# Performance work log

Hardware: AMD Instinct MI355X
Metric: run time of the kernel (lower is better)

The kernel has to match this reference:

```python
import jax, jax.numpy as jnp
import numpy as np

NEG_SLOPE = 0.2


def _gat(x, edge_index, W, a_src, a_dst, b):
    """PyG-style GATConv, heads=1, add_self_loops=True."""
    n = x.shape[0]
    x = x @ W  # [n, out]
    loops = jnp.arange(n, dtype=edge_index.dtype)
    src = jnp.concatenate([edge_index[0], loops])
    dst = jnp.concatenate([edge_index[1], loops])
    a_s = x @ a_src  # [n]
    a_d = x @ a_dst  # [n]
    e = jax.nn.leaky_relu(a_s[src] + a_d[dst], NEG_SLOPE)  # [E]
    m = jax.ops.segment_max(e, dst, num_segments=n)  # stable softmax per dst
    ex = jnp.exp(e - m[dst])
    denom = jax.ops.segment_sum(ex, dst, num_segments=n)
    alpha = ex / denom[dst]
    out = jax.ops.segment_sum(alpha[:, None] * x[src], dst, num_segments=n)
    return out + b


def _lin(key, fan_in, fan_out):
    k1, k2 = jax.random.split(key)
    s = 1.0 / np.sqrt(fan_in)
    W = jax.random.uniform(k1, (fan_in, fan_out), jnp.float32, -s, s)
    b = jax.random.uniform(k2, (fan_out,), jnp.float32, -s, s)
    return W, b


def setup_inputs() -> dict:
    key = jax.random.key(0)
    ks = jax.random.split(key, 24)
    ND, FD = 50000, 128   # drug nodes / feat dim
    NC, FC = 10000, 735   # cell nodes / feat dim
    ED, EC = 800000, 160000
    B = 16384
    inp = {}
    inp['drug_x'] = jax.random.normal(ks[0], (ND, FD), jnp.float32)
    inp['cell_x'] = jax.random.normal(ks[1], (NC, FC), jnp.float32)
    inp['drug_edge_index'] = jax.random.randint(ks[2], (2, ED), 0, ND, jnp.int64 if jax.config.jax_enable_x64 else jnp.int32)
    inp['cell_edge_index'] = jax.random.randint(ks[3], (2, EC), 0, NC, jnp.int32)
    inp['drug_indices'] = jax.random.randint(ks[4], (B,), 0, ND, jnp.int32)
    inp['cell_indices'] = jax.random.randint(ks[5], (B,), 0, NC, jnp.int32)
    # drug feature transform: Linear(128,256)
    inp['dW1'], inp['db1'] = _lin(ks[6], FD, 256)
    # cell feature transform: Linear(735,1024) -> Linear(1024,256)
    inp['cW1'], inp['cb1'] = _lin(ks[7], FC, 1024)
    inp['cW2'], inp['cb2'] = _lin(ks[8], 1024, 256)
    # drug GAT (256->256)
    inp['gdW'], _ = _lin(ks[9], 256, 256)
    inp['gdas'] = jax.random.normal(ks[10], (256,), jnp.float32) * 0.1
    inp['gdad'] = jax.random.normal(ks[11], (256,), jnp.float32) * 0.1
    inp['gdb'] = jnp.zeros((256,), jnp.float32)
    # cell GAT1 (256->1024)
    inp['g1W'], _ = _lin(ks[12], 256, 1024)
    inp['g1as'] = jax.random.normal(ks[13], (1024,), jnp.float32) * 0.1
    inp['g1ad'] = jax.random.normal(ks[14], (1024,), jnp.float32) * 0.1
    inp['g1b'] = jnp.zeros((1024,), jnp.float32)
    # cell GAT2 (1024->256)
    inp['g2W'], _ = _lin(ks[15], 1024, 256)
    inp['g2as'] = jax.random.normal(ks[16], (256,), jnp.float32) * 0.1
    inp['g2ad'] = jax.random.normal(ks[17], (256,), jnp.float32) * 0.1
    inp['g2b'] = jnp.zeros((256,), jnp.float32)
    inp['rW1'], inp['rb1'] = _lin(ks[18], 512, 512)
    inp['rW2'], inp['rb2'] = _lin(ks[19], 512, 512)
    inp['rW3'], inp['rb3'] = _lin(ks[20], 512, 1)
    return inp


def reference(drug_x, cell_x, drug_edge_index, cell_edge_index, drug_indices, cell_indices,
              dW1, db1, cW1, cb1, cW2, cb2,
              gdW, gdas, gdad, gdb,
              g1W, g1as, g1ad, g1b,
              g2W, g2as, g2ad, g2b,
              rW1, rb1, rW2, rb2, rW3, rb3):
    # feature transforms (dropout = identity in eval mode)
    d = jax.nn.relu(drug_x @ dW1 + db1)                 # [ND, 256]
    c = jax.nn.relu(cell_x @ cW1 + cb1)                 # [NC, 1024]
    c = jax.nn.relu(c @ cW2 + cb2)                      # [NC, 256]
    # GAT layers
    d = jax.nn.relu(_gat(d, drug_edge_index, gdW, gdas, gdad, gdb))   # [ND, 256]
    c = jax.nn.relu(_gat(c, cell_edge_index, g1W, g1as, g1ad, g1b))   # [NC, 1024]
    c = jax.nn.relu(_gat(c, cell_edge_index, g2W, g2as, g2ad, g2b))   # [NC, 256]
    comb = jnp.concatenate([d[drug_indices], c[cell_indices]], axis=-1)  # [B, 512]
    h = jax.nn.elu(comb @ rW1 + rb1)
    h = jax.nn.elu(h @ rW2 + rb2)
    return h @ rW3 + rb3                                 # [B, 1]
```

## Files before the change

kernel.cpp:

```cpp
#include <hip/hip_runtime.h>
#include <math.h>

#define NEG_SLOPE 0.2f

typedef __attribute__((ext_vector_type(8))) short short8;
typedef __attribute__((ext_vector_type(4))) float floatx4;

__device__ __forceinline__ unsigned short f2bf(float f) {
    unsigned u = __float_as_uint(f);
    u += 0x7fffu + ((u >> 16) & 1u);
    return (unsigned short)(u >> 16);
}
__device__ __forceinline__ float bf2f(unsigned short h) {
    return __uint_as_float((unsigned)h << 16);
}
__device__ __forceinline__ float lrelu(float v) {
    return v > 0.f ? v : NEG_SLOPE * v;
}

typedef __attribute__((address_space(3))) unsigned int lds_u32;
typedef const __attribute__((address_space(1))) unsigned int glb_u32c;
__device__ __forceinline__ void gll16(const unsigned short* g, unsigned short* l) {
    __builtin_amdgcn_global_load_lds((glb_u32c*)g, (lds_u32*)l, 16, 0, 0);
}

struct SJob { const float* W; unsigned short* Th; unsigned short* Tl; int K, N, Kp, base; };
struct SJobs { SJob j[8]; };

__global__ __launch_bounds__(256) void split_transpose_multi(SJobs js) {
    int t = blockIdx.x;
    int ji = 0;
#pragma unroll
    for (int q = 1; q < 8; ++q) if (t >= js.j[q].base) ji = q;
    const SJob jb = js.j[ji];
    int local = t - jb.base;
    int ntiles = jb.N / 32;
    int tn = local % ntiles, tk = local / ntiles;
    int k0 = tk * 32, n0 = tn * 32;
    __shared__ float tbuf[32][33];
    int c = threadIdx.x & 31, r = threadIdx.x >> 5;
    for (int rr = r; rr < 32; rr += 8) {
        int k = k0 + rr, n = n0 + c;
        tbuf[rr][c] = (k < jb.K && n < jb.N) ? jb.W[(long)k * jb.N + n] : 0.f;
    }
    __syncthreads();
    for (int rr = r; rr < 32; rr += 8) {
        int n = n0 + rr, k = k0 + c;
        if (n < jb.N && k < jb.Kp) {
            float v = tbuf[c][rr];
            unsigned short h = f2bf(v);
            jb.Th[(long)n * jb.Kp + k] = h;
            jb.Tl[(long)n * jb.Kp + k] = f2bf(v - bf2f(h));
        }
    }
}

__global__ __launch_bounds__(256) void split_cell_rows(
    const float* __restrict__ X, unsigned short* __restrict__ H,
    unsigned short* __restrict__ L, int M)
{
    long i = blockIdx.x;
    int t = threadIdx.x;
    const float* r = X + i * 735;
    for (int c = t; c < 736; c += 256) {
        float v = (c < 735) ? r[c] : 0.f;
        unsigned short h = f2bf(v);
        H[i * 736 + c] = h;
        L[i * 736 + c] = f2bf(v - bf2f(h));
    }
}

__global__ __launch_bounds__(256) void matvec4(
    const float* __restrict__ gdW, const float* __restrict__ gdas, const float* __restrict__ gdad,
    float* __restrict__ wds, float* __restrict__ wdd,
    const float* __restrict__ g1W, const float* __restrict__ g1as, const float* __restrict__ g1ad,
    float* __restrict__ w1s, float* __restrict__ w1d)
{
    int b = blockIdx.x;
    int sel = b >> 8, k = b & 255, t = threadIdx.x;
    const float *W, *a; float* o; int N;
    if (sel == 0)      { W = gdW; a = gdas; o = wds; N = 256; }
    else if (sel == 1) { W = gdW; a = gdad; o = wdd; N = 256; }
    else if (sel == 2) { W = g1W; a = g1as; o = w1s; N = 1024; }
    else               { W = g1W; a = g1ad; o = w1d; N = 1024; }
    float s = 0.f;
    for (int n = t; n < N; n += 256) s += W[(long)k * N + n] * a[n];
#pragma unroll
    for (int off = 32; off; off >>= 1) s += __shfl_down(s, off);
    __shared__ float ls[4];
    if ((t & 63) == 0) ls[t >> 6] = s;
    __syncthreads();
    if (t == 0) o[k] = ls[0] + ls[1] + ls[2] + ls[3];
}

__global__ __launch_bounds__(256, 3) void gemm_d0_fused(
    const float* __restrict__ A,
    const unsigned short* __restrict__ Bh_g,
    const unsigned short* __restrict__ Bl_g,
    const float* __restrict__ bias,
    const float* __restrict__ was, const float* __restrict__ wad,
    float* __restrict__ C,
    float* __restrict__ das, float* __restrict__ dad,
    int M, int nblk)
{
    int bid = blockIdx.x;
    int q = nblk >> 3, rr = nblk & 7;
    int xcd = bid & 7, idx = bid >> 3;
    int wg = (xcd < rr ? xcd * (q + 1) : rr * (q + 1) + (xcd - rr) * q) + idx;
    int rb = wg >> 1, colh = wg & 1;
    int m0 = rb * 64, n0 = colh * 128;
    if (m0 >= M) return;
    const int tid = threadIdx.x;
    const int wave = tid >> 6, lane = tid & 63;
    const int lm = lane & 15, lq = lane >> 4;
    const int wn = n0 + wave * 32;

    floatx4 acc[4][2];
    floatx4 zero = {0.f, 0.f, 0.f, 0.f};
#pragma unroll
    for (int i = 0; i < 4; ++i)
#pragma unroll
        for (int j = 0; j < 2; ++j) acc[i][j] = zero;

#pragma unroll
    for (int ks = 0; ks < 4; ++ks) {
        const int kc = ks * 32 + lq * 8;
        short8 bh[2], bl[2];
#pragma unroll
        for (int j = 0; j < 2; ++j) {
            long bo = (long)(wn + j * 16 + lm) * 128 + kc;
            bh[j] = *(const short8*)(Bh_g + bo);
            bl[j] = *(const short8*)(Bl_g + bo);
        }
        short8 ah[4], al[4];
#pragma unroll
        for (int i = 0; i < 4; ++i) {
            int gm = m0 + i * 16 + lm;
            float4 t0 = {0.f, 0.f, 0.f, 0.f}, t1 = {0.f, 0.f, 0.f, 0.f};
            if (gm < M) {
                const float* ap = A + (long)gm * 128 + kc;
                t0 = *(const float4*)ap;
                t1 = *(const float4*)(ap + 4);
            }
            short8 h, l;
            float f;
            f = t0.x; h[0] = f2bf(f); l[0] = f2bf(f - bf2f(h[0]));
            f = t0.y; h[1] = f2bf(f); l[1] = f2bf(f - bf2f(h[1]));
            f = t0.z; h[2] = f2bf(f); l[2] = f2bf(f - bf2f(h[2]));
            f = t0.w; h[3] = f2bf(f); l[3] = f2bf(f - bf2f(h[3]));
            f = t1.x; h[4] = f2bf(f); l[4] = f2bf(f - bf2f(h[4]));
            f = t1.y; h[5] = f2bf(f); l[5] = f2bf(f - bf2f(h[5]));
            f = t1.z; h[6] = f2bf(f); l[6] = f2bf(f - bf2f(h[6]));
            f = t1.w; h[7] = f2bf(f); l[7] = f2bf(f - bf2f(h[7]));
            ah[i] = h; al[i] = l;
        }
#pragma unroll
        for (int i = 0; i < 4; ++i)
#pragma unroll
            for (int j = 0; j < 2; ++j) {
                acc[i][j] = __builtin_amdgcn_mfma_f32_16x16x32_bf16(ah[i], bh[j], acc[i][j], 0, 0, 0);
                acc[i][j] = __builtin_amdgcn_mfma_f32_16x16x32_bf16(al[i], bh[j], acc[i][j], 0, 0, 0);
                acc[i][j] = __builtin_amdgcn_mfma_f32_16x16x32_bf16(ah[i], bl[j], acc[i][j], 0, 0, 0);
            }
    }

    __shared__ float sps[64][5], spd[64][5];
    float bv[2], wsv[2], wdv[2];
#pragma unroll
    for (int j = 0; j < 2; ++j) {
        int gn = wn + j * 16 + lm;
        bv[j] = bias[gn];
        wsv[j] = was[gn];
        wdv[j] = wad[gn];
    }
#pragma unroll
    for (int i = 0; i < 4; ++i) {
#pragma unroll
        for (int r = 0; r < 4; ++r) {
            int gm = m0 + i * 16 + lq * 4 + r;
            float vs = 0.f, vd = 0.f;
#pragma unroll
            for (int j = 0; j < 2; ++j) {
                int gn = wn + j * 16 + lm;
                float v = fmaxf(acc[i][j][r] + bv[j], 0.f);
                if (gm < M) C[(long)gm * 256 + gn] = v;
                vs = fmaf(v, wsv[j], vs);
                vd = fmaf(v, wdv[j], vd);
            }
#pragma unroll
            for (int o = 8; o; o >>= 1) {
                vs += __shfl_xor(vs, o);
                vd += __shfl_xor(vd, o);
            }
            if (lm == 0) {
                sps[i * 16 + lq * 4 + r][wave] = vs;
                spd[i * 16 + lq * 4 + r][wave] = vd;
            }
        }
    }
    __syncthreads();
    if (tid < 64) {
        int gm = m0 + tid;
        if (gm < M) {
            float s = sps[tid][0] + sps[tid][1] + sps[tid][2] + sps[tid][3];
            float d2 = spd[tid][0] + spd[tid][1] + spd[tid][2] + spd[tid][3];
            atomicAdd(das + gm, s);
            atomicAdd(dad + gm, d2);
        }
    }
}

template<int ACT, int OSPLIT>
__global__ __launch_bounds__(256, 6) void gemm2(
    const unsigned short* __restrict__ Ah_g, const unsigned short* __restrict__ Al_g,
    const unsigned short* __restrict__ Bh_g, const unsigned short* __restrict__ Bl_g,
    const float* __restrict__ bias,
    float* __restrict__ C, unsigned short* __restrict__ Ch_g, unsigned short* __restrict__ Cl_g,
    int M, int K, int N, int Kp, int Cs)
{
    __shared__ unsigned short Ah[2048];
    __shared__ unsigned short Al[2048];
    __shared__ unsigned short Bh[4096];
    __shared__ unsigned short Bl[4096];
    const int tid = threadIdx.x;
    const int wave = tid >> 6, lane = tid & 63;
    const int lm = lane & 15, lq = lane >> 4;
    const int wn = wave * 32;
    const int nx = gridDim.x;
    const int lin = blockIdx.y * nx + blockIdx.x;
    const int sup = lin / (8 * nx);
    const int wit = lin - sup * 8 * nx;
    const int rowb = sup * 8 + (wit & 7);
    const int nb = wit >> 3;
    const int m0 = rowb * 64, n0 = nb * 128;
    if (m0 >= M) return;

    floatx4 acc[4][2];
    floatx4 zero = {0.f, 0.f, 0.f, 0.f};
#pragma unroll
    for (int i = 0; i < 4; ++i)
#pragma unroll
        for (int j = 0; j < 2; ++j) acc[i][j] = zero;

    const int srow = lane >> 2;
    const int sslot = (lane & 3) ^ ((lane >> 3) & 3);
    const unsigned short* agh = Ah_g + (long)(m0 + wave * 16 + srow) * Kp + sslot * 8;
    const unsigned short* agl = Al_g + (long)(m0 + wave * 16 + srow) * Kp + sslot * 8;
    const unsigned short* bgh0 = Bh_g + (long)(n0 + wave * 32 + srow) * Kp + sslot * 8;
    const unsigned short* bgh1 = Bh_g + (long)(n0 + wave * 32 + 16 + srow) * Kp + sslot * 8;
    const unsigned short* bgl0 = Bl_g + (long)(n0 + wave * 32 + srow) * Kp + sslot * 8;
    const unsigned short* bgl1 = Bl_g + (long)(n0 + wave * 32 + 16 + srow) * Kp + sslot * 8;
    unsigned short* lAh = &Ah[wave * 512];
    unsigned short* lAl = &Al[wave * 512];
    unsigned short* lBh0 = &Bh[wave * 1024];
    unsigned short* lBh1 = &Bh[wave * 1024 + 512];
    unsigned short* lBl0 = &Bl[wave * 1024];
    unsigned short* lBl1 = &Bl[wave * 1024 + 512];
    const int xa = (lm >> 1) & 3;

    for (int k0 = 0; k0 < K; k0 += 32) {
        gll16(agh + k0, lAh);
        gll16(agl + k0, lAl);
        gll16(bgh0 + k0, lBh0);
        gll16(bgh1 + k0, lBh1);
        gll16(bgl0 + k0, lBl0);
        gll16(bgl1 + k0, lBl1);
        __syncthreads();
        short8 fah[4], fal[4], fbh[2], fbl[2];
#pragma unroll
        for (int i = 0; i < 4; ++i) {
            int off = (i * 16 + lm) * 32 + ((lq ^ xa) << 3);
            fah[i] = *(const short8*)&Ah[off];
            fal[i] = *(const short8*)&Al[off];
        }
#pragma unroll
        for (int j = 0; j < 2; ++j) {
            int off = (wn + j * 16 + lm) * 32 + ((lq ^ xa) << 3);
            fbh[j] = *(const short8*)&Bh[off];
            fbl[j] = *(const short8*)&Bl[off];
        }
#pragma unroll
        for (int i = 0; i < 4; ++i)
#pragma unroll
            for (int j = 0; j < 2; ++j) {
                acc[i][j] = __builtin_amdgcn_mfma_f32_16x16x32_bf16(fah[i], fbh[j], acc[i][j], 0, 0, 0);
                acc[i][j] = __builtin_amdgcn_mfma_f32_16x16x32_bf16(fal[i], fbh[j], acc[i][j], 0, 0, 0);
                acc[i][j] = __builtin_amdgcn_mfma_f32_16x16x32_bf16(fah[i], fbl[j], acc[i][j], 0, 0, 0);
            }
        __syncthreads();
    }
#pragma unroll
    for (int j = 0; j < 2; ++j) {
        int gn = n0 + wn + j * 16 + lm;
        float bv = bias ? bias[gn] : 0.f;
#pragma unroll
        for (int i = 0; i < 4; ++i) {
#pragma unroll
            for (int r = 0; r < 4; ++r) {
                int gm = m0 + i * 16 + lq * 4 + r;
                if (gm < M) {
                    float v = acc[i][j][r] + bv;
                    if (ACT == 1) v = fmaxf(v, 0.f);
                    if (ACT == 2) v = v > 0.f ? v : expm1f(v);
                    if (OSPLIT) {
                        long o = (long)gm * Cs + gn;
                        unsigned short h = f2bf(v);
                        Ch_g[o] = h;
                        Cl_g[o] = f2bf(v - bf2f(h));
                    } else {
                        C[(long)gm * (long)Cs + gn] = v;
                    }
                }
            }
        }
    }
}

__global__ __launch_bounds__(256) void att_scalars(
    const float* __restrict__ x, const float* __restrict__ avs,
    const float* __restrict__ avd, float* __restrict__ outs,
    float* __restrict__ outd, int F)
{
    const int i = blockIdx.x;
    const int t = threadIdx.x;
    float ps = 0.f, pd = 0.f;
    for (int f = t; f < F; f += 256) {
        float v = x[(long)i * F + f];
        ps += v * avs[f];
        pd += v * avd[f];
    }
#pragma unroll
    for (int off = 32; off; off >>= 1) {
        ps += __shfl_down(ps, off);
        pd += __shfl_down(pd, off);
    }
    __shared__ float ls[4], ld[4];
    int lane = t & 63, w = t >> 6;
    if (lane == 0) { ls[w] = ps; ld[w] = pd; }
    __syncthreads();
    if (t == 0) {
        outs[i] = ls[0] + ls[1] + ls[2] + ls[3];
        outd[i] = ld[0] + ld[1] + ld[2] + ld[3];
    }
}

__global__ __launch_bounds__(256) void hist_kernel(
    const int* __restrict__ dst, int* __restrict__ cnt, int E, int n)
{
    int t = blockIdx.x * 256 + threadIdx.x;
    if (t >= E + n) return;
    int d = t < E ? dst[t] : (t - E);
    atomicAdd(&cnt[d], 1);
}

__global__ __launch_bounds__(256) void scan1_kernel(
    const int* __restrict__ cnt, int* __restrict__ off,
    int* __restrict__ bsum, int n)
{
    __shared__ int s[256];
    int b = blockIdx.x, t = threadIdx.x, i = b * 256 + t;
    int v = (i < n) ? cnt[i] : 0;
    s[t] = v;
    __syncthreads();
    for (int d = 1; d < 256; d <<= 1) {
        int u = (t >= d) ? s[t - d] : 0;
        __syncthreads();
        s[t] += u;
        __syncthreads();
    }
    if (i < n) off[i] = s[t] - v;
    if (t == 255) bsum[b] = s[255];
}

__global__ __launch_bounds__(256) void scan2_kernel(
    const int* __restrict__ bsum, int* __restrict__ bpre, int nb,
    int* __restrict__ off, int n)
{
    __shared__ int s[256];
    int t = threadIdx.x;
    int v = (t < nb) ? bsum[t] : 0;
    s[t] = v;
    __syncthreads();
    for (int d = 1; d < 256; d <<= 1) {
        int u = (t >= d) ? s[t - d] : 0;
        __syncthreads();
        s[t] += u;
        __syncthreads();
    }
    if (t < nb) bpre[t] = s[t] - v;
    if (t == 255) off[n] = s[255];
}

__global__ __launch_bounds__(256) void scan3_kernel(
    int* __restrict__ off, int* __restrict__ cursor,
    const int* __restrict__ bpre, int n)
{
    int i = blockIdx.x * 256 + threadIdx.x;
    if (i < n) {
        int v = off[i] + bpre[blockIdx.x];
        off[i] = v;
        cursor[i] = v;
    }
}

__global__ __launch_bounds__(256) void scatter_kernel(
    const int* __restrict__ src, const int* __restrict__ dst,
    int* __restrict__ cursor, int* __restrict__ ebuf, int E, int n)
{
    int t = blockIdx.x * 256 + threadIdx.x;
    if (t >= E + n) return;
    int s = t < E ? src[t] : (t - E);
    int d = t < E ? dst[t] : (t - E);
    int pos = atomicAdd(&cursor[d], 1);
    ebuf[pos] = s;
}

template<int EPI>
__global__ __launch_bounds__(256) void gat_agg3(
    const int* __restrict__ off, const int* __restrict__ ebuf,
    const float* __restrict__ as_, const float* __restrict__ ad_,
    const float* __restrict__ x, const float* __restrict__ bias,
    const int* __restrict__ dmap,
    float* __restrict__ outF, unsigned short* __restrict__ outH,
    unsigned short* __restrict__ outL, int nrows)
{
    int row = blockIdx.x * 4 + (threadIdx.x >> 6);
    int lane = threadIdx.x & 63;
    if (row >= nrows) return;
    int d = dmap ? dmap[row] : row;
    int lo = off[d], hi = off[d + 1];
    float adv = ad_[d];

    float m = -INFINITY;
    for (int p = lo + lane; p < hi; p += 64)
        m = fmaxf(m, lrelu(as_[ebuf[p]] + adv));
#pragma unroll
    for (int o = 32; o; o >>= 1) m = fmaxf(m, __shfl_xor(m, o));

    const float* xb = x + lane * 4;
    float4 acc = {0.f, 0.f, 0.f, 0.f};
    float psum = 0.f;
    for (int base = lo; base < hi; base += 64) {
        int cnt = min(64, hi - base);
        int s = 0;
        float ex = 0.f;
        if (lane < cnt) {
            s = ebuf[base + lane];
            ex = expf(lrelu(as_[s] + adv) - m);
        }
        psum += ex;
        for (int i = 0; i < cnt; ++i) {
            int si = __shfl(s, i);
            float ei = __shfl(ex, i);
            float4 v = *(const float4*)(xb + (long)si * 256);
            acc.x = fmaf(ei, v.x, acc.x);
            acc.y = fmaf(ei, v.y, acc.y);
            acc.z = fmaf(ei, v.z, acc.z);
            acc.w = fmaf(ei, v.w, acc.w);
        }
    }
#pragma unroll
    for (int o = 32; o; o >>= 1) psum += __shfl_xor(psum, o);
    float inv = 1.f / psum;

    long ob = (long)row * 256 + lane * 4;
    if (EPI == 1) {
        float r0 = fmaxf(acc.x * inv + bias[lane * 4 + 0], 0.f);
        float r1 = fmaxf(acc.y * inv + bias[lane * 4 + 1], 0.f);
        float r2 = fmaxf(acc.z * inv + bias[lane * 4 + 2], 0.f);
        float r3 = fmaxf(acc.w * inv + bias[lane * 4 + 3], 0.f);
        float4 r = {r0, r1, r2, r3};
        *(float4*)(outF + ob) = r;
    } else {
        float vv[4] = {acc.x * inv, acc.y * inv, acc.z * inv, acc.w * inv};
#pragma unroll
        for (int j = 0; j < 4; ++j) {
            unsigned short h = f2bf(vv[j]);
            outH[ob + j] = h;
            outL[ob + j] = f2bf(vv[j] - bf2f(h));
        }
    }
}

__global__ __launch_bounds__(256) void gather_cell_split(
    const float* __restrict__ cfin, const int* __restrict__ cidx,
    unsigned short* __restrict__ combH, unsigned short* __restrict__ combL)
{
    int i = blockIdx.x;
    int t = threadIdx.x;
    float v = cfin[(long)cidx[i] * 256 + t];
    long b = (long)i * 512 + 256 + t;
    unsigned short h = f2bf(v);
    combH[b] = h;
    combL[b] = f2bf(v - bf2f(h));
}

__global__ __launch_bounds__(256) void head_final_kernel(
    const float* __restrict__ h, const float* __restrict__ w,
    const float* __restrict__ b, float* __restrict__ out, int M)
{
    int gw = blockIdx.x * 4 + (threadIdx.x >> 6);
    int lane = threadIdx.x & 63;
    if (gw >= M) return;
    const float* row = h + (long)gw * 512;
    float s = 0.f;
#pragma unroll
    for (int f = lane; f < 512; f += 64) s += row[f] * w[f];
#pragma unroll
    for (int off = 32; off; off >>= 1) s += __shfl_down(s, off);
    if (lane == 0) out[gw] = s + b[0];
}

static inline dim3 mfma_grid64(int M, int N) {
    int ny = (M + 63) / 64;
    ny = (ny + 7) & ~7;
    return dim3(N / 128, ny);
}

extern "C" void kernel_launch(void* const* d_in, const int* in_sizes, int n_in,
                              void* d_out, int out_size, void* d_ws, size_t ws_size,
                              hipStream_t stream)
{
    const float* drug_x = (const float*)d_in[0];
    const float* cell_x = (const float*)d_in[1];
    const int* d_ei = (const int*)d_in[2];
    const int* c_ei = (const int*)d_in[3];
    const int* d_idx = (const int*)d_in[4];
    const int* c_idx = (const int*)d_in[5];
    const float* dW1 = (const float*)d_in[6];
    const float* db1 = (const float*)d_in[7];
    const float* cW1 = (const float*)d_in[8];
    const float* cb1 = (const float*)d_in[9];
    const float* cW2 = (const float*)d_in[10];
    const float* cb2 = (const float*)d_in[11];
    const float* gdW = (const float*)d_in[12];
    const float* gdas = (const float*)d_in[13];
    const float* gdad = (const float*)d_in[14];
    const float* gdb = (const float*)d_in[15];
    const float* g1W = (const float*)d_in[16];
    const float* g1as = (const float*)d_in[17];
    const float* g1ad = (const float*)d_in[18];
    const float* g1b = (const float*)d_in[19];
    const float* g2W = (const float*)d_in[20];
    const float* g2as = (const float*)d_in[21];
    const float* g2ad = (const float*)d_in[22];
    const float* g2b = (const float*)d_in[23];
    const float* rW1 = (const float*)d_in[24];
    const float* rb1 = (const float*)d_in[25];
    const float* rW2 = (const float*)d_in[26];
    const float* rb2 = (const float*)d_in[27];
    const float* rW3 = (const float*)d_in[28];
    const float* rb3 = (const float*)d_in[29];

    const int ND = in_sizes[0] / 128;
    const int NC = in_sizes[1] / 735;
    const int ED = in_sizes[2] / 2;
    const int EC = in_sizes[3] / 2;
    const int NB = in_sizes[4];

    const int* d_src = d_ei;
    const int* d_dst = d_ei + ED;
    const int* c_src = c_ei;
    const int* c_dst = c_ei + EC;

    const size_t MB = 1ull << 20;
    const size_t KB = 1024;
    char* ws = (char*)d_ws;

    size_t wo = 0;
    auto walloc = [&](size_t elems) -> unsigned short* {
        unsigned short* p = (unsigned short*)(ws + wo);
        wo += ((elems * 2 + 255) & ~(size_t)255);
        return p;
    };
    unsigned short* dW1h = walloc(256 * 128);  unsigned short* dW1l = walloc(256 * 128);
    unsigned short* cW1h = walloc(1024 * 736); unsigned short* cW1l = walloc(1024 * 736);
    unsigned short* cW2h = walloc(256 * 1024); unsigned short* cW2l = walloc(256 * 1024);
    unsigned short* gdWh = walloc(256 * 256);  unsigned short* gdWl = walloc(256 * 256);
    unsigned short* g1Wh = walloc(1024 * 256); unsigned short* g1Wl = walloc(1024 * 256);
    unsigned short* g2Wh = walloc(256 * 1024); unsigned short* g2Wl = walloc(256 * 1024);
    unsigned short* rW1h = walloc(512 * 512);  unsigned short* rW1l = walloc(512 * 512);
    unsigned short* rW2h = walloc(512 * 512);  unsigned short* rW2l = walloc(512 * 512);

    float* wa_ds  = (float*)(ws + 9 * MB);
    float* wa_dd  = (float*)(ws + 9 * MB + 4 * KB);
    float* wa_c1s = (float*)(ws + 9 * MB + 8 * KB);
    float* wa_c1d = (float*)(ws + 9 * MB + 12 * KB);
    float* cas    = (float*)(ws + 9 * MB + 64 * KB);
    float* cad    = (float*)(ws + 9 * MB + 128 * KB);
    int*   coff   = (int*)(ws + 9 * MB + 192 * KB);
    int*   ccur   = (int*)(ws + 9 * MB + 256 * KB);
    int*   ccnt   = (int*)(ws + 9 * MB + 320 * KB);
    int*   bsum_d = (int*)(ws + 9 * MB + 400 * KB);
    int*   bpre_d = (int*)(ws + 9 * MB + 404 * KB);
    int*   bsum_c = (int*)(ws + 9 * MB + 408 * KB);
    int*   bpre_c = (int*)(ws + 9 * MB + 412 * KB);
    int*   cebuf  = (int*)(ws + 10 * MB);
    float* das    = (float*)(ws + 11 * MB);
    float* dad    = (float*)(ws + 11 * MB + 256 * KB);
    int*   doff   = (int*)(ws + 11 * MB + 512 * KB);
    int*   dcur   = (int*)(ws + 11 * MB + 768 * KB);
    int*   dcnt   = (int*)(ws + 12 * MB);
    int*   debuf  = (int*)(ws + 12 * MB + 256 * KB);

    float* dbuf  = (float*)(ws + 16 * MB);
    unsigned short* aggdh = (unsigned short*)(ws + 66 * MB);
    unsigned short* aggdl = (unsigned short*)(ws + 75 * MB);
    unsigned short* combh = (unsigned short*)(ws + 84 * MB);
    unsigned short* combl = (unsigned short*)(ws + 101 * MB);
    unsigned short* c0h = (unsigned short*)(ws + 16 * MB);
    unsigned short* c0l = (unsigned short*)(ws + 36 * MB);
    float* c1b   = (float*)(ws + 118 * MB);
    unsigned short* aggch = (unsigned short*)(ws + 129 * MB);
    unsigned short* aggcl = (unsigned short*)(ws + 135 * MB);
    unsigned short* c2h = (unsigned short*)(ws + 16 * MB);
    unsigned short* c2l = (unsigned short*)(ws + 36 * MB);
    float* xc2   = (float*)(ws + 118 * MB);
    float* cfin  = (float*)(ws + 141 * MB);
    unsigned short* h1h = (unsigned short*)(ws + 16 * MB);
    unsigned short* h1l = (unsigned short*)(ws + 33 * MB);
    float* h2b   = (float*)(ws + 50 * MB);
    unsigned short* cxh = (unsigned short*)(ws + 152 * MB);
    unsigned short* cxl = (unsigned short*)(ws + 167 * MB);

    SJobs js;
    js.j[0] = {dW1, dW1h, dW1l, 128, 256, 128, 0};
    js.j[1] = {cW1, cW1h, cW1l, 735, 1024, 736, 32};
    js.j[2] = {cW2, cW2h, cW2l, 1024, 256, 1024, 768};
    js.j[3] = {gdW, gdWh, gdWl, 256, 256, 256, 1024};
    js.j[4] = {g1W, g1Wh, g1Wl, 256, 1024, 256, 1088};
    js.j[5] = {g2W, g2Wh, g2Wl, 1024, 256, 1024, 1344};
    js.j[6] = {rW1, rW1h, rW1l, 512, 512, 512, 1600};
    js.j[7] = {rW2, rW2h, rW2l, 512, 512, 512, 1856};
    split_transpose_multi<<<2112, 256, 0, stream>>>(js);
    split_cell_rows<<<NC, 256, 0, stream>>>(cell_x, cxh, cxl, NC);
    matvec4<<<1024, 256, 0, stream>>>(gdW, gdas, gdad, wa_ds, wa_dd,
                                      g1W, g1as, g1ad, wa_c1s, wa_c1d);

    hipMemsetAsync(das, 0, (size_t)ND * 4, stream);
    hipMemsetAsync(dad, 0, (size_t)ND * 4, stream);
    {
        int nblk = 2 * ((ND + 63) / 64);
        gemm_d0_fused<<<nblk, 256, 0, stream>>>(
            drug_x, dW1h, dW1l, db1, wa_ds, wa_dd, dbuf, das, dad, ND, nblk);
    }
    hipMemsetAsync(dcnt, 0, (size_t)ND * 4, stream);
    {
        int tot = ED + ND;
        int nbd = (ND + 255) / 256;
        hist_kernel<<<(tot + 255) / 256, 256, 0, stream>>>(d_dst, dcnt, ED, ND);
        scan1_kernel<<<nbd, 256, 0, stream>>>(dcnt, doff, bsum_d, ND);
        scan2_kernel<<<1, 256, 0, stream>>>(bsum_d, bpre_d, nbd, doff, ND);
        scan3_kernel<<<nbd, 256, 0, stream>>>(doff, dcur, bpre_d, ND);
        scatter_kernel<<<(tot + 255) / 256, 256, 0, stream>>>(d_src, d_dst, dcur, debuf, ED, ND);
        gat_agg3<0><<<(NB + 3) / 4, 256, 0, stream>>>(doff, debuf, das, dad, dbuf, nullptr,
                                                      d_idx, nullptr, aggdh, aggdl, NB);
    }
    gemm2<1, 1><<<mfma_grid64(NB, 256), 256, 0, stream>>>(
        aggdh, aggdl, gdWh, gdWl, gdb, nullptr, combh, combl,
        NB, 256, 256, 256, 512);

    gemm2<1, 1><<<mfma_grid64(NC, 1024), 256, 0, stream>>>(
        cxh, cxl, cW1h, cW1l, cb1, nullptr, c0h, c0l,
        NC, 736, 1024, 736, 1024);
    gemm2<1, 0><<<mfma_grid64(NC, 256), 256, 0, stream>>>(
        c0h, c0l, cW2h, cW2l, cb2, c1b, nullptr, nullptr,
        NC, 1024, 256, 1024, 256);
    att_scalars<<<NC, 256, 0, stream>>>(c1b, wa_c1s, wa_c1d, cas, cad, 256);
    hipMemsetAsync(ccnt, 0, (size_t)NC * 4, stream);
    {
        int tot = EC + NC;
        int nbc = (NC + 255) / 256;
        hist_kernel<<<(tot + 255) / 256, 256, 0, stream>>>(c_dst, ccnt, EC, NC);
        scan1_kernel<<<nbc, 256, 0, stream>>>(ccnt, coff, bsum_c, NC);
        scan2_kernel<<<1, 256, 0, stream>>>(bsum_c, bpre_c, nbc, coff, NC);
        scan3_kernel<<<nbc, 256, 0, stream>>>(coff, ccur, bpre_c, NC);
        scatter_kernel<<<(tot + 255) / 256, 256, 0, stream>>>(c_src, c_dst, ccur, cebuf, EC, NC);
        gat_agg3<0><<<(NC + 3) / 4, 256, 0, stream>>>(coff, cebuf, cas, cad, c1b, nullptr,
                                                      nullptr, nullptr, aggch, aggcl, NC);
    }
    gemm2<1, 1><<<mfma_grid64(NC, 1024), 256, 0, stream>>>(
        aggch, aggcl, g1Wh, g1Wl, g1b, nullptr, c2h, c2l,
        NC, 256, 1024, 256, 1024);
    gemm2<0, 0><<<mfma_grid64(NC, 256), 256, 0, stream>>>(
        c2h, c2l, g2Wh, g2Wl, nullptr, xc2, nullptr, nullptr,
        NC, 1024, 256, 1024, 256);
    att_scalars<<<NC, 256, 0, stream>>>(xc2, g2as, g2ad, cas, cad, 256);
    gat_agg3<1><<<(NC + 3) / 4, 256, 0, stream>>>(coff, cebuf, cas, cad, xc2, g2b,
                                                  nullptr, cfin, nullptr, nullptr, NC);

    gather_cell_split<<<NB, 256, 0, stream>>>(cfin, c_idx, combh, combl);
    gemm2<2, 1><<<mfma_grid64(NB, 512), 256, 0, stream>>>(
        combh, combl, rW1h, rW1l, rb1, nullptr, h1h, h1l,
        NB, 512, 512, 512, 512);
    gemm2<2, 0><<<mfma_grid64(NB, 512), 256, 0, stream>>>(
        h1h, h1l, rW2h, rW2l, rb2, h2b, nullptr, nullptr,
        NB, 512, 512, 512, 512);
    head_final_kernel<<<(NB + 3) / 4, 256, 0, stream>>>(h2b, rW3, rb3, (float*)d_out, NB);
}
```

Measured before the change: 747.7 us.

## Fuse attention scalars and head dot into GEMM epilogues; merge graph CSR builds

Adds template flags to the GEMM epilogue so the attention source/destination dot products and the final regression dot product are computed in-register, shuffle-reduced and atomically accumulated. This removes the att_scalars and head_final kernels and the re-reads of intermediate buffers. The drug and cell CSR construction (histogram, three scan stages, scatter) is merged into single launches, the workspace is relaid out so one memset clears the counters, and the cell gather is vectorized to four rows per block. Float atomics make the accumulation order nondeterministic, and the output must be zeroed first.

```diff
diff --git a/kernel.cpp b/kernel.cpp
--- a/kernel.cpp
+++ b/kernel.cpp
@@ -210,12 +210,15 @@
     }
 }
 
-template<int ACT, int OSPLIT>
+template<int ACT, int OSPLIT, int FATT, int HDOT>
 __global__ __launch_bounds__(256, 6) void gemm2(
     const unsigned short* __restrict__ Ah_g, const unsigned short* __restrict__ Al_g,
     const unsigned short* __restrict__ Bh_g, const unsigned short* __restrict__ Bl_g,
     const float* __restrict__ bias,
     float* __restrict__ C, unsigned short* __restrict__ Ch_g, unsigned short* __restrict__ Cl_g,
+    const float* __restrict__ was, const float* __restrict__ wad,
+    float* __restrict__ oas, float* __restrict__ oad,
+    const float* __restrict__ hw, const float* __restrict__ hb, float* __restrict__ hout,
     int M, int K, int N, int Kp, int Cs)
 {
     __shared__ unsigned short Ah[2048];
@@ -289,19 +292,27 @@
             }
         __syncthreads();
     }
+    float bv[2], wsv[2], wdv[2], hwv[2];
 #pragma unroll
     for (int j = 0; j < 2; ++j) {
         int gn = n0 + wn + j * 16 + lm;
-        float bv = bias ? bias[gn] : 0.f;
-#pragma unroll
-        for (int i = 0; i < 4; ++i) {
-#pragma unroll
-            for (int r = 0; r < 4; ++r) {
-                int gm = m0 + i * 16 + lq * 4 + r;
-                if (gm < M) {
-                    float v = acc[i][j][r] + bv;
-                    if (ACT == 1) v = fmaxf(v, 0.f);
-                    if (ACT == 2) v = v > 0.f ? v : expm1f(v);
+        bv[j] = bias ? bias[gn] : 0.f;
+        if (FATT) { wsv[j] = was[gn]; wdv[j] = wad[gn]; }
+        if (HDOT) { hwv[j] = hw[gn]; }
+    }
+#pragma unroll
+    for (int i = 0; i < 4; ++i) {
+#pragma unroll
+        for (int r = 0; r < 4; ++r) {
+            int gm = m0 + i * 16 + lq * 4 + r;
+            float vs = 0.f, vd = 0.f, hp = 0.f;
+#pragma unroll
+            for (int j = 0; j < 2; ++j) {
+                int gn = n0 + wn + j * 16 + lm;
+                float v = acc[i][j][r] + bv[j];
+                if (ACT == 1) v = fmaxf(v, 0.f);
+                if (ACT == 2) v = v > 0.f ? v : expm1f(v);
+                if (!HDOT && gm < M) {
                     if (OSPLIT) {
                         long o = (long)gm * Cs + gn;
                         unsigned short h = f2bf(v);
@@ -311,54 +322,56 @@
                         C[(long)gm * (long)Cs + gn] = v;
                     }
                 }
-            }
-        }
-    }
-}
-
-__global__ __launch_bounds__(256) void att_scalars(
-    const float* __restrict__ x, const float* __restrict__ avs,
-    const float* __restrict__ avd, float* __restrict__ outs,
-    float* __restrict__ outd, int F)
-{
-    const int i = blockIdx.x;
-    const int t = threadIdx.x;
-    float ps = 0.f, pd = 0.f;
-    for (int f = t; f < F; f += 256) {
-        float v = x[(long)i * F + f];
-        ps += v * avs[f];
-        pd += v * avd[f];
-    }
-#pragma unroll
-    for (int off = 32; off; off >>= 1) {
-        ps += __shfl_down(ps, off);
-        pd += __shfl_down(pd, off);
-    }
-    __shared__ float ls[4], ld[4];
-    int lane = t & 63, w = t >> 6;
-    if (lane == 0) { ls[w] = ps; ld[w] = pd; }
-    __syncthreads();
-    if (t == 0) {
-        outs[i] = ls[0] + ls[1] + ls[2] + ls[3];
-        outd[i] = ld[0] + ld[1] + ld[2] + ld[3];
-    }
-}
-
-__global__ __launch_bounds__(256) void hist_kernel(
-    const int* __restrict__ dst, int* __restrict__ cnt, int E, int n)
+                if (FATT) { vs = fmaf(v, wsv[j], vs); vd = fmaf(v, wdv[j], vd); }
+                if (HDOT) { hp = fmaf(v, hwv[j], hp); }
+            }
+            if (FATT) {
+#pragma unroll
+                for (int o = 8; o; o >>= 1) {
+                    vs += __shfl_xor(vs, o);
+                    vd += __shfl_xor(vd, o);
+                }
+                if (lm == 0 && gm < M) {
+                    atomicAdd(oas + gm, vs);
+                    atomicAdd(oad + gm, vd);
+                }
+            }
+            if (HDOT) {
+#pragma unroll
+                for (int o = 8; o; o >>= 1) hp += __shfl_xor(hp, o);
+                if (lm == 0 && gm < M) {
+                    float add = hp;
+                    if (n0 == 0 && wave == 0) add += hb[0];
+                    atomicAdd(hout + gm, add);
+                }
+            }
+        }
+    }
+}
+
+__global__ __launch_bounds__(256) void hist2_kernel(
+    const int* __restrict__ ddst, int* __restrict__ dcnt, int ED, int ND,
+    const int* __restrict__ cdst, int* __restrict__ ccnt, int EC, int NC)
 {
     int t = blockIdx.x * 256 + threadIdx.x;
-    if (t >= E + n) return;
-    int d = t < E ? dst[t] : (t - E);
-    atomicAdd(&cnt[d], 1);
-}
-
-__global__ __launch_bounds__(256) void scan1_kernel(
-    const int* __restrict__ cnt, int* __restrict__ off,
-    int* __restrict__ bsum, int n)
+    int tot1 = ED + ND;
+    if (t < tot1) {
+        int d = t < ED ? ddst[t] : (t - ED);
+        atomicAdd(&dcnt[d], 1);
+    } else {
+        int u = t - tot1;
+        if (u < EC + NC) {
+            int d = u < EC ? cdst[u] : (u - EC);
+            atomicAdd(&ccnt[d], 1);
+        }
+    }
+}
+
+__device__ __forceinline__ void scan1_body(
+    const int* cnt, int* off, int* bsum, int n, int b, int t)
 {
     __shared__ int s[256];
-    int b = blockIdx.x, t = threadIdx.x, i = b * 256 + t;
+    int i = b * 256 + t;
     int v = (i < n) ? cnt[i] : 0;
     s[t] = v;
     __syncthreads();
@@ -372,12 +385,19 @@
     if (t == 255) bsum[b] = s[255];
 }
 
-__global__ __launch_bounds__(256) void scan2_kernel(
-    const int* __restrict__ bsum, int* __restrict__ bpre, int nb,
-    int* __restrict__ off, int n)
+__global__ __launch_bounds__(256) void scan1both_kernel(
+    const int* __restrict__ dcnt, int* __restrict__ doff, int* __restrict__ bsum_d, int ND, int nbd,
+    const int* __restrict__ ccnt, int* __restrict__ coff, int* __restrict__ bsum_c, int NC)
+{
+    int b = blockIdx.x, t = threadIdx.x;
+    if (b < nbd) scan1_body(dcnt, doff, bsum_d, ND, b, t);
+    else         scan1_body(ccnt, coff, bsum_c, NC, b - nbd, t);
+}
+
+__device__ __forceinline__ void scan2_body(
+    const int* bsum, int* bpre, int nb, int* off, int n, int t)
 {
     __shared__ int s[256];
-    int t = threadIdx.x;
     int v = (t < nb) ? bsum[t] : 0;
     s[t] = v;
     __syncthreads();
@@ -391,28 +411,59 @@
     if (t == 255) off[n] = s[255];
 }
 
-__global__ __launch_bounds__(256) void scan3_kernel(
-    int* __restrict__ off, int* __restrict__ cursor,
-    const int* __restrict__ bpre, int n)
-{
-    int i = blockIdx.x * 256 + threadIdx.x;
-    if (i < n) {
-        int v = off[i] + bpre[blockIdx.x];
-        off[i] = v;
-        cursor[i] = v;
-    }
-}
-
-__global__ __launch_bounds__(256) void scatter_kernel(
-    const int* __restrict__ src, const int* __restrict__ dst,
-    int* __restrict__ cursor, int* __restrict__ ebuf, int E, int n)
+__global__ __launch_bounds__(256) void scan2both_kernel(
+    const int* __restrict__ bsum_d, int* __restrict__ bpre_d, int nbd, int* __restrict__ doff, int ND,
+    const int* __restrict__ bsum_c, int* __restrict__ bpre_c, int nbc, int* __restrict__ coff, int NC)
+{
+    int t = threadIdx.x;
+    if (blockIdx.x == 0) scan2_body(bsum_d, bpre_d, nbd, doff, ND, t);
+    else                 scan2_body(bsum_c, bpre_c, nbc, coff, NC, t);
+}
+
+__global__ __launch_bounds__(256) void scan3both_kernel(
+    int* __restrict__ doff, int* __restrict__ dcur, const int* __restrict__ bpre_d, int ND, int nbd,
+    int* __restrict__ coff, int* __restrict__ ccur, const int* __restrict__ bpre_c, int NC)
+{
+    int b = blockIdx.x, t = threadIdx.x;
+    if (b < nbd) {
+        int i = b * 256 + t;
+        if (i < ND) {
+            int v = doff[i] + bpre_d[b];
+            doff[i] = v;
+            dcur[i] = v;
+        }
+    } else {
+        int i = (b - nbd) * 256 + t;
+        if (i < NC) {
+            int v = coff[i] + bpre_c[b - nbd];
+            coff[i] = v;
+            ccur[i] = v;
+        }
+    }
+}
+
+__global__ __launch_bounds__(256) void scatter2_kernel(
+    const int* __restrict__ dsrc, const int* __restrict__ ddst,
+    int* __restrict__ dcur, int* __restrict__ debuf, int ED, int ND,
+    const int* __restrict__ csrc, const int* __restrict__ cdst,
+    int* __restrict__ ccur, int* __restrict__ cebuf, int EC, int NC)
 {
     int t = blockIdx.x * 256 + threadIdx.x;
-    if (t >= E + n) return;
-    int s = t < E ? src[t] : (t - E);
-    int d = t < E ? dst[t] : (t - E);
-    int pos = atomicAdd(&cursor[d], 1);
-    ebuf[pos] = s;
+    int tot1 = ED + ND;
+    if (t < tot1) {
+        int s = t < ED ? dsrc[t] : (t - ED);
+        int d = t < ED ? ddst[t] : (t - ED);
+        int pos = atomicAdd(&dcur[d], 1);
+        debuf[pos] = s;
+    } else {
+        int u = t - tot1;
+        if (u < EC + NC) {
+            int s = u < EC ? csrc[u] : (u - EC);
+            int d = u < EC ? cdst[u] : (u - EC);
+            int pos = atomicAdd(&ccur[d], 1);
+            cebuf[pos] = s;
+        }
+    }
 }
 
 template<int EPI>
@@ -482,33 +533,21 @@
     }
 }
 
-__global__ __launch_bounds__(256) void gather_cell_split(
+__global__ __launch_bounds__(256) void gather_cell_split4(
     const float* __restrict__ cfin, const int* __restrict__ cidx,
     unsigned short* __restrict__ combH, unsigned short* __restrict__ combL)
 {
-    int i = blockIdx.x;
-    int t = threadIdx.x;
-    float v = cfin[(long)cidx[i] * 256 + t];
-    long b = (long)i * 512 + 256 + t;
-    unsigned short h = f2bf(v);
-    combH[b] = h;
-    combL[b] = f2bf(v - bf2f(h));
-}
-
-__global__ __launch_bounds__(256) void head_final_kernel(
-    const float* __restrict__ h, const float* __restrict__ w,
-    const float* __restrict__ b, float* __restrict__ out, int M)
-{
-    int gw = blockIdx.x * 4 + (threadIdx.x >> 6);
+    int row = blockIdx.x * 4 + (threadIdx.x >> 6);
     int lane = threadIdx.x & 63;
-    if (gw >= M) return;
-    const float* row = h + (long)gw * 512;
-    float s = 0.f;
-#pragma unroll
-    for (int f = lane; f < 512; f += 64) s += row[f] * w[f];
-#pragma unroll
-    for (int off = 32; off; off >>= 1) s += __shfl_down(s, off);
-    if (lane == 0) out[gw] = s + b[0];
+    float4 v = *(const float4*)(cfin + (long)cidx[row] * 256 + lane * 4);
+    long b = (long)row * 512 + 256 + lane * 4;
+    float vv[4] = {v.x, v.y, v.z, v.w};
+#pragma unroll
+    for (int j = 0; j < 4; ++j) {
+        unsigned short h = f2bf(vv[j]);
+        combH[b + j] = h;
+        combL[b + j] = f2bf(vv[j] - bf2f(h));
+    }
 }
 
 static inline dim3 mfma_grid64(int M, int N) {
@@ -586,22 +625,22 @@
     float* wa_dd  = (float*)(ws + 9 * MB + 4 * KB);
     float* wa_c1s = (float*)(ws + 9 * MB + 8 * KB);
     float* wa_c1d = (float*)(ws + 9 * MB + 12 * KB);
-    float* cas    = (float*)(ws + 9 * MB + 64 * KB);
-    float* cad    = (float*)(ws + 9 * MB + 128 * KB);
-    int*   coff   = (int*)(ws + 9 * MB + 192 * KB);
-    int*   ccur   = (int*)(ws + 9 * MB + 256 * KB);
-    int*   ccnt   = (int*)(ws + 9 * MB + 320 * KB);
     int*   bsum_d = (int*)(ws + 9 * MB + 400 * KB);
     int*   bpre_d = (int*)(ws + 9 * MB + 404 * KB);
     int*   bsum_c = (int*)(ws + 9 * MB + 408 * KB);
     int*   bpre_c = (int*)(ws + 9 * MB + 412 * KB);
+    int*   doff   = (int*)(ws + 9 * MB + 448 * KB);
+    int*   dcur   = (int*)(ws + 9 * MB + 704 * KB);
     int*   cebuf  = (int*)(ws + 10 * MB);
+    int*   coff   = (int*)(ws + 10 * MB + 768 * KB);
+    int*   ccur   = (int*)(ws + 10 * MB + 832 * KB);
     float* das    = (float*)(ws + 11 * MB);
     float* dad    = (float*)(ws + 11 * MB + 256 * KB);
-    int*   doff   = (int*)(ws + 11 * MB + 512 * KB);
-    int*   dcur   = (int*)(ws + 11 * MB + 768 * KB);
-    int*   dcnt   = (int*)(ws + 12 * MB);
-    int*   debuf  = (int*)(ws + 12 * MB + 256 * KB);
+    int*   dcnt   = (int*)(ws + 11 * MB + 512 * KB);
+    int*   ccnt   = (int*)(ws + 11 * MB + 768 * KB);
+    float* cas    = (float*)(ws + 11 * MB + 832 * KB);
+    float* cad    = (float*)(ws + 11 * MB + 896 * KB);
+    int*   debuf  = (int*)(ws + 12 * MB);
 
     float* dbuf  = (float*)(ws + 16 * MB);
     unsigned short* aggdh = (unsigned short*)(ws + 66 * MB);
@@ -619,9 +658,11 @@
     float* cfin  = (float*)(ws + 141 * MB);
     unsigned short* h1h = (unsigned short*)(ws + 16 * MB);
     unsigned short* h1l = (unsigned short*)(ws + 33 * MB);
-    float* h2b   = (float*)(ws + 50 * MB);
     unsigned short* cxh = (unsigned short*)(ws + 152 * MB);
     unsigned short* cxl = (unsigned short*)(ws + 167 * MB);
+
+    hipMemsetAsync(ws + 11 * MB, 0, 960 * KB, stream);
+    hipMemsetAsync(d_out, 0, (size_t)NB * 4, stream);
 
     SJobs js;
     js.j[0] = {dW1, dW1h, dW1l, 128, 256, 128, 0};
@@ -637,64 +678,63 @@
     matvec4<<<1024, 256, 0, stream>>>(gdW, gdas, gdad, wa_ds, wa_dd,
                                       g1W, g1as, g1ad, wa_c1s, wa_c1d);
 
-    hipMemsetAsync(das, 0, (size_t)ND * 4, stream);
-    hipMemsetAsync(dad, 0, (size_t)ND * 4, stream);
+    {
+        int nbd = (ND + 255) / 256, nbc = (NC + 255) / 256;
+        int tot = (ED + ND) + (EC + NC);
+        hist2_kernel<<<(tot + 255) / 256, 256, 0, stream>>>(
+            d_dst, dcnt, ED, ND, c_dst, ccnt, EC, NC);
+        scan1both_kernel<<<nbd + nbc, 256, 0, stream>>>(
+            dcnt, doff, bsum_d, ND, nbd, ccnt, coff, bsum_c, NC);
+        scan2both_kernel<<<2, 256, 0, stream>>>(
+            bsum_d, bpre_d, nbd, doff, ND, bsum_c, bpre_c, nbc, coff, NC);
+        scan3both_kernel<<<nbd + nbc, 256, 0, stream>>>(
+            doff, dcur, bpre_d, ND, nbd, coff, ccur, bpre_c, NC);
+        scatter2_kernel<<<(tot + 255) / 256, 256, 0, stream>>>(
+            d_src, d_dst, dcur, debuf, ED, ND,
+            c_src, c_dst, ccur, cebuf, EC, NC);
+    }
+
     {
         int nblk = 2 * ((ND + 63) / 64);
         gemm_d0_fused<<<nblk, 256, 0, stream>>>(
             drug_x, dW1h, dW1l, db1, wa_ds, wa_dd, dbuf, das, dad, ND, nblk);
     }
-    hipMemsetAsync(dcnt, 0, (size_t)ND * 4, stream);
-    {
-        int tot = ED + ND;
-        int nbd = (ND + 255) / 256;
-        hist_kernel<<<(tot + 255) / 256, 256, 0, stream>>>(d_dst, dcnt, ED, ND);
-        scan1_kernel<<<nbd, 256, 0, stream>>>(dcnt, doff, bsum_d, ND);
-        scan2_kernel<<<1, 256, 0, stream>>>(bsum_d, bpre_d, nbd, doff, ND);
-        scan3_kernel<<<nbd, 256, 0, stream>>>(doff, dcur, bpre_d, ND);
-        scatter_kernel<<<(tot + 255) / 256, 256, 0, stream>>>(d_src, d_dst, dcur, debuf, ED, ND);
-        gat_agg3<0><<<(NB + 3) / 4, 256, 0, stream>>>(doff, debuf, das, dad, dbuf, nullptr,
-                                                      d_idx, nullptr, aggdh, aggdl, NB);
-    }
-    gemm2<1, 1><<<mfma_grid64(NB, 256), 256, 0, stream>>>(
+    gat_agg3<0><<<(NB + 3) / 4, 256, 0, stream>>>(doff, debuf, das, dad, dbuf, nullptr,
+                                                  d_idx, nullptr, aggdh, aggdl, NB);
+    gemm2<1, 1, 0, 0><<<mfma_grid64(NB, 256), 256, 0, stream>>>(
         aggdh, aggdl, gdWh, gdWl, gdb, nullptr, combh, combl,
+        nullptr, nullptr, nullptr, nullptr, nullptr, nullptr, nullptr,
         NB, 256, 256, 256, 512);
 
-    gemm2<1, 1><<<mfma_grid64(NC, 1024), 256, 0, stream>>>(
+    gemm2<1, 1, 0, 0><<<mfma_grid64(NC, 1024), 256, 0, stream>>>(
         cxh, cxl, cW1h, cW1l, cb1, nullptr, c0h, c0l,
+        nullptr, nullptr, nullptr, nullptr, nullptr, nullptr, nullptr,
         NC, 736, 1024, 736, 1024);
-    gemm2<1, 0><<<mfma_grid64(NC, 256), 256, 0, stream>>>(
+    gemm2<1, 0, 1, 0><<<mfma_grid64(NC, 256), 256, 0, stream>>>(
         c0h, c0l, cW2h, cW2l, cb2, c1b, nullptr, nullptr,
+        wa_c1s, wa_c1d, cas, cad, nullptr, nullptr, nullptr,
         NC, 1024, 256, 1024, 256);
-    att_scalars<<<NC, 256, 0, stream>>>(c1b, wa_c1s, wa_c1d, cas, cad, 256);
-    hipMemsetAsync(ccnt, 0, (size_t)NC * 4, stream);
-    {
-        int tot = EC + NC;
-        int nbc = (NC + 255) / 256;
-        hist_kernel<<<(tot + 255) / 256, 256, 0, stream>>>(c_dst, ccnt, EC, NC);
-        scan1_kernel<<<nbc, 256, 0, stream>>>(ccnt, coff, bsum_c, NC);
-        scan2_kernel<<<1, 256, 0, stream>>>(bsum_c, bpre_c, nbc, coff, NC);
-        scan3_kernel<<<nbc, 256, 0, stream>>>(coff, ccur, bpre_c, NC);
-        scatter_kernel<<<(tot + 255) / 256, 256, 0, stream>>>(c_src, c_dst, ccur, cebuf, EC, NC);
-        gat_agg3<0><<<(NC + 3) / 4, 256, 0, stream>>>(coff, cebuf, cas, cad, c1b, nullptr,
-                                                      nullptr, nullptr, aggch, aggcl, NC);
-    }
-    gemm2<1, 1><<<mfma_grid64(NC, 1024), 256, 0, stream>>>(
+    gat_agg3<0><<<(NC + 3) / 4, 256, 0, stream>>>(coff, cebuf, cas, cad, c1b, nullptr,
+                                                  nullptr, nullptr, aggch, aggcl, NC);
+    gemm2<1, 1, 0, 0><<<mfma_grid64(NC, 1024), 256, 0, stream>>>(
         aggch, aggcl, g1Wh, g1Wl, g1b, nullptr, c2h, c2l,
+        nullptr, nullptr, nullptr, nullptr, nullptr, nullptr, nullptr,
         NC, 256, 1024, 256, 1024);
-    gemm2<0, 0><<<mfma_grid64(NC, 256), 256, 0, stream>>>(
+    hipMemsetAsync(ws + 11 * MB + 832 * KB, 0, 128 * KB, stream);
+    gemm2<0, 0, 1, 0><<<mfma_grid64(NC, 256), 256, 0, stream>>>(
         c2h, c2l, g2Wh, g2Wl, nullptr, xc2, nullptr, nullptr,
+        g2as, g2ad, cas, cad, nullptr, nullptr, nullptr,
         NC, 1024, 256, 1024, 256);
-    att_scalars<<<NC, 256, 0, stream>>>(xc2, g2as, g2ad, cas, cad, 256);
     gat_agg3<1><<<(NC + 3) / 4, 256, 0, stream>>>(coff, cebuf, cas, cad, xc2, g2b,
                                                   nullptr, cfin, nullptr, nullptr, NC);
 
-    gather_cell_split<<<NB, 256, 0, stream>>>(cfin, c_idx, combh, combl);
-    gemm2<2, 1><<<mfma_grid64(NB, 512), 256, 0, stream>>>(
+    gather_cell_split4<<<NB / 4, 256, 0, stream>>>(cfin, c_idx, combh, combl);
+    gemm2<2, 1, 0, 0><<<mfma_grid64(NB, 512), 256, 0, stream>>>(
         combh, combl, rW1h, rW1l, rb1, nullptr, h1h, h1l,
+        nullptr, nullptr, nullptr, nullptr, nullptr, nullptr, nullptr,
         NB, 512, 512, 512, 512);
-    gemm2<2, 0><<<mfma_grid64(NB, 512), 256, 0, stream>>>(
-        h1h, h1l, rW2h, rW2l, rb2, h2b, nullptr, nullptr,
+    gemm2<2, 0, 0, 1><<<mfma_grid64(NB, 512), 256, 0, stream>>>(
+        h1h, h1l, rW2h, rW2l, rb2, nullptr, nullptr, nullptr,
+        nullptr, nullptr, nullptr, nullptr, rW3, rb3, (float*)d_out,
         NB, 512, 512, 512, 512);
-    head_final_kernel<<<(NB + 3) / 4, 256, 0, stream>>>(h2b, rW3, rb3, (float*)d_out, NB);
-}
+}
```

After: 688.8 us. 1.09x faster.
